# Performance work log

Hardware: AMD Instinct MI355X
Metric: run time of the kernel (lower is better)

Reference implementation:

```python
import jax, jax.numpy as jnp
import numpy as np
import math

D_MODEL = 768
N_HEADS = 12
B, L = 2, 2048
ALPHA = 0.3

def setup_inputs() -> dict:
    key = jax.random.key(0)
    ks = jax.random.split(key, 7)
    s = 0.02
    return {
        "x": jax.random.normal(ks[0], (B, L, D_MODEL), dtype=jnp.float32),
        "Wqkv_w": jax.random.normal(ks[1], (D_MODEL, 3 * D_MODEL), dtype=jnp.float32) * s,
        "Wqkv_b": jax.random.normal(ks[2], (3 * D_MODEL,), dtype=jnp.float32) * s,
        "sel_w": jax.random.normal(ks[3], (D_MODEL, 2), dtype=jnp.float32) * s,
        "sel_b": jax.random.normal(ks[4], (2,), dtype=jnp.float32) * s,
        "out_w": jax.random.normal(ks[5], (D_MODEL, D_MODEL), dtype=jnp.float32) * s,
        "out_b": jax.random.normal(ks[6], (D_MODEL,), dtype=jnp.float32) * s,
        "temperature": jnp.ones((1,), dtype=jnp.float32) * (math.sqrt(D_MODEL) * ALPHA),
    }

def reference(x, Wqkv_w, Wqkv_b, sel_w, sel_b, out_w, out_b, temperature):
    b, l, d = x.shape
    h = N_HEADS
    hd = d // h
    # QKV projection: (B, L, 3, H, hd)
    qkv = (x @ Wqkv_w + Wqkv_b).reshape(b, l, 3, h, hd)
    q, k_, v = qkv[:, :, 0], qkv[:, :, 1], qkv[:, :, 2]
    scale = 1.0 / math.sqrt(hd)
    scores = jnp.einsum('bthd,bshd->bhts', q, k_ * scale)  # (B,H,L,L)
    causal_mask = jnp.triu(jnp.full((l, l), -10000.0, dtype=scores.dtype), 1)
    attn = jax.nn.softmax(scores + causal_mask, axis=-1)
    ctx = jnp.einsum('bhts,bshd->bthd', attn, v).reshape(b, l, d)
    attn_output = ctx @ out_w + out_b  # (B,L,D)
    # selection gate: softmax over 2 logits, keep prob of class 1 -> (B,L,1)
    selection = jax.nn.softmax((x @ sel_w + sel_b) / temperature, axis=-1)[..., 1:]
    # eval-mode top-k routing
    k_sel = int(math.ceil(math.sqrt(l)))
    _, idx = jax.lax.top_k(selection[..., 0], k_sel)  # (B, k)
    gated = attn_output * selection  # (B,L,D)
    src = jnp.take_along_axis(gated, idx[..., None], axis=1)  # (B,k,D)
    y = jax.vmap(lambda xb, ib, sb: xb.at[ib].add(sb))(x, idx, src)
    return y
```

## Files before the change

kernel.cpp:

```cpp
#include <hip/hip_runtime.h>
#include <hip/hip_bf16.h>
#include <cstddef>

#define BATCH 2
#define SEQ   2048
#define DM    768
#define NH    12
#define HD    64
#define N3    2304
#define NKV   1536
#define KSEL  46
#define NROW  (BATCH*KSEL)
#define NCHUNK 32

typedef unsigned short ushort_t;
typedef __attribute__((ext_vector_type(8))) short bf16x8;
typedef __attribute__((ext_vector_type(4))) float f32x4;

__device__ __forceinline__ ushort_t f2bf(float f) {
  union { __hip_bfloat16 h; ushort_t u; } cv;
  cv.h = __float2bfloat16(f);
  return cv.u;
}
__device__ __forceinline__ float bf2f(ushort_t u) {
  union { unsigned int i; float f; } cv;
  cv.i = ((unsigned int)u) << 16;
  return cv.f;
}

#define GLD16(g, l)                                                         \
  __builtin_amdgcn_global_load_lds(                                         \
      (const __attribute__((address_space(1))) void*)(g),                   \
      (__attribute__((address_space(3))) void*)(l), 16, 0, 0)

__global__ __launch_bounds__(256) void prep_kernel(
    const float* __restrict__ x, const float* __restrict__ W,
    const float* __restrict__ Wo,
    const float* __restrict__ sel_w, const float* __restrict__ sel_b,
    const float* __restrict__ temp,
    ushort_t* __restrict__ xb, ushort_t* __restrict__ Wt,
    ushort_t* __restrict__ WoT,
    float* __restrict__ sel, float* __restrict__ y) {
  const int bx = blockIdx.x;
  const int tid = threadIdx.x;
  if (bx < 1024) {
    const int w = tid >> 6, lane = tid & 63;
    const int row = bx * 4 + w;
    const float4* xr4 = (const float4*)(x + (size_t)row * DM);
    float4* yr4 = (float4*)(y + (size_t)row * DM);
    ushort4* xb4 = (ushort4*)(xb + (size_t)row * DM);
    const float4* sw4 = (const float4*)sel_w;
    float a0 = 0.f, a1 = 0.f;
#pragma unroll
    for (int i = 0; i < 3; ++i) {
      const int p = i * 64 + lane;
      float4 f = xr4[p];
      yr4[p] = f;
      ushort4 o;
      o.x = f2bf(f.x); o.y = f2bf(f.y); o.z = f2bf(f.z); o.w = f2bf(f.w);
      xb4[p] = o;
      float4 sa = sw4[p * 2];
      float4 sb = sw4[p * 2 + 1];
      a0 += f.x * sa.x + f.y * sa.z + f.z * sb.x + f.w * sb.z;
      a1 += f.x * sa.y + f.y * sa.w + f.z * sb.y + f.w * sb.w;
    }
    for (int off = 32; off; off >>= 1) {
      a0 += __shfl_xor(a0, off);
      a1 += __shfl_xor(a1, off);
    }
    if (lane == 0) {
      float t = temp[0];
      float l0 = (a0 + sel_b[0]) / t;
      float l1 = (a1 + sel_b[1]) / t;
      sel[row] = 1.0f / (1.0f + expf(l0 - l1));
    }
  } else if (bx < 2752) {
    __shared__ float tile[32][33];
    const int bx2 = bx - 1024;
    const int n0 = (bx2 % 72) * 32, k0 = (bx2 / 72) * 32;
    const int r = tid >> 3, c4 = (tid & 7) * 4;
    float4 f = *(const float4*)&W[(size_t)(k0 + r) * N3 + n0 + c4];
    tile[r][c4] = f.x; tile[r][c4 + 1] = f.y; tile[r][c4 + 2] = f.z; tile[r][c4 + 3] = f.w;
    __syncthreads();
    ushort4 o;
    o.x = f2bf(tile[c4 + 0][r]);
    o.y = f2bf(tile[c4 + 1][r]);
    o.z = f2bf(tile[c4 + 2][r]);
    o.w = f2bf(tile[c4 + 3][r]);
    *(ushort4*)&Wt[(size_t)(n0 + r) * DM + k0 + c4] = o;
  } else {
    __shared__ float tile2[32][33];
    const int bx3 = bx - 2752;
    const int n0 = (bx3 % 24) * 32, k0 = (bx3 / 24) * 32;
    const int r = tid >> 3, c4 = (tid & 7) * 4;
    float4 f = *(const float4*)&Wo[(size_t)(k0 + r) * DM + n0 + c4];
    tile2[r][c4] = f.x; tile2[r][c4 + 1] = f.y; tile2[r][c4 + 2] = f.z; tile2[r][c4 + 3] = f.w;
    __syncthreads();
    ushort4 o;
    o.x = f2bf(tile2[c4 + 0][r]);
    o.y = f2bf(tile2[c4 + 1][r]);
    o.z = f2bf(tile2[c4 + 2][r]);
    o.w = f2bf(tile2[c4 + 3][r]);
    *(ushort4*)&WoT[(size_t)(n0 + r) * DM + k0 + c4] = o;
  }
}

__global__ __launch_bounds__(256) void topk_kernel(
    const float* __restrict__ sel, int* __restrict__ idx,
    int* __restrict__ idxp) {
  __shared__ unsigned int hist[256];
  __shared__ unsigned int cum[256];
  __shared__ unsigned int wtot[4];
  __shared__ int sh_b;
  __shared__ int c_gt, c_eq;
  __shared__ int tmp_gt[KSEL];
  __shared__ int eqlist[256];
  __shared__ int fin[64];
  __shared__ int srt[64];
  const int b = blockIdx.x, tid = threadIdx.x;
  const int lane = tid & 63, w = tid >> 6;

  unsigned int key[8];
  int  kidx[8];
#pragma unroll
  for (int e = 0; e < 8; ++e) {
    int i = e * 256 + tid;
    kidx[e] = i;
    key[e] = __float_as_uint(sel[b * SEQ + i]);
  }
  unsigned int prefix = 0, mask = 0;
  int r = KSEL;
#pragma unroll
  for (int p = 3; p >= 0; --p) {
    const int shift = 8 * p;
    hist[tid] = 0;
    __syncthreads();
#pragma unroll
    for (int e = 0; e < 8; ++e)
      if ((key[e] & mask) == prefix)
        atomicAdd(&hist[(key[e] >> shift) & 255], 1u);
    __syncthreads();
    unsigned int v = hist[tid];
#pragma unroll
    for (int off = 1; off < 64; off <<= 1) {
      unsigned int t = __shfl_down(v, off);
      if (lane + off < 64) v += t;
    }
    if (lane == 0) wtot[w] = v;
    __syncthreads();
    unsigned int addhi = 0;
    for (int ww = w + 1; ww < 4; ++ww) addhi += wtot[ww];
    v += addhi;
    cum[tid] = v;
    __syncthreads();
    if (v >= (unsigned int)r && (tid == 255 || cum[tid + 1] < (unsigned int)r))
      sh_b = tid;
    __syncthreads();
    const int bsel = sh_b;
    r -= (bsel == 255) ? 0 : (int)cum[bsel + 1];
    prefix |= ((unsigned int)bsel) << shift;
    mask |= 0xFFu << shift;
    __syncthreads();
  }
  if (tid == 0) { c_gt = 0; c_eq = 0; }
  __syncthreads();
#pragma unroll
  for (int e = 0; e < 8; ++e) {
    if (key[e] > prefix) {
      int pos = atomicAdd(&c_gt, 1);
      tmp_gt[pos] = kidx[e];
    } else if (key[e] == prefix) {
      int pos = atomicAdd(&c_eq, 1);
      if (pos < 256) eqlist[pos] = kidx[e];
    }
  }
  __syncthreads();
  if (tid == 0) {
    const int need = KSEL - c_gt;
    const int ec = (c_eq < 256) ? c_eq : 256;
    for (int a = 0; a < need; ++a) {
      int mb = a;
      for (int bb = a + 1; bb < ec; ++bb)
        if (eqlist[bb] < eqlist[mb]) mb = bb;
      int tv = eqlist[a]; eqlist[a] = eqlist[mb]; eqlist[mb] = tv;
    }
  }
  __syncthreads();
  if (tid < KSEL)
    fin[tid] = (tid < c_gt) ? tmp_gt[tid] : eqlist[tid - c_gt];
  __syncthreads();
  if (tid < KSEL) {
    const int v = fin[tid];
    int rank = 0;
    for (int j = 0; j < KSEL; ++j) rank += (fin[j] < v);
    srt[rank] = v;
  }
  __syncthreads();
  if (tid < 64) {
    if (tid < KSEL) {
      idx[b * KSEL + tid] = srt[tid];
      idxp[b * 64 + tid] = srt[tid];
    } else {
      idxp[b * 64 + tid] = 0;
    }
  }
}

__global__ __launch_bounds__(256) void gemm_kernel(
    const ushort_t* __restrict__ Xbf,
    const ushort_t* __restrict__ Wt,
    const float* __restrict__ bias,
    const int* __restrict__ idxp,
    ushort_t* __restrict__ Ckv,
    ushort_t* __restrict__ qb) {
  __shared__ ushort_t As[128 * 32];
  __shared__ ushort_t Bs[64 * 32];
  const int bid = blockIdx.x;
  const int tid = threadIdx.x;
  const int lane = tid & 63, w = tid >> 6;
  const int wr = w >> 1, wc = w & 1;
  const int quad = lane >> 4, l16 = lane & 15;
  const int ci0 = tid;
  const int ci1 = 256 + tid;
  const bool isQ = (bid >= 768);
  int m0, nw0;
  size_t ga0, ga1;
  if (isQ) {
    m0 = 0;
    nw0 = (bid - 768) * 64;
    const int r0 = ci0 >> 2, r1 = ci1 >> 2;
    ga0 = (size_t)((r0 >> 6) * SEQ + idxp[r0]) * DM;
    ga1 = (size_t)((r1 >> 6) * SEQ + idxp[r1]) * DM;
  } else {
    const int bid2 = (bid & 7) * 96 + (bid >> 3);
    m0 = (bid2 / 24) * 128;
    nw0 = 768 + (bid2 % 24) * 64;
    ga0 = (size_t)(m0 + (ci0 >> 2)) * DM;
    ga1 = (size_t)(m0 + (ci1 >> 2)) * DM;
  }
  const size_t gb0 = (size_t)(nw0 + (tid >> 2)) * DM;
  const int ka0 = (ci0 & 3) * 8, ka1 = (ci1 & 3) * 8;
  const int kq = (tid & 3) * 8;

  f32x4 acc[4][2] = {};
  for (int k0 = 0; k0 < DM; k0 += 32) {
    GLD16(Xbf + ga0 + k0 + ka0, &As[(w * 64) * 8]);
    GLD16(Xbf + ga1 + k0 + ka1, &As[(256 + w * 64) * 8]);
    GLD16(Wt + gb0 + k0 + kq, &Bs[(w * 16) * 32]);
    __syncthreads();
    bf16x8 af[4], bfr[2];
#pragma unroll
    for (int i = 0; i < 4; ++i)
      af[i] = *(const bf16x8*)&As[(wr * 64 + i * 16 + l16) * 32 + quad * 8];
#pragma unroll
    for (int j = 0; j < 2; ++j)
      bfr[j] = *(const bf16x8*)&Bs[(wc * 32 + j * 16 + l16) * 32 + quad * 8];
#pragma unroll
    for (int i = 0; i < 4; ++i)
#pragma unroll
      for (int j = 0; j < 2; ++j)
        acc[i][j] = __builtin_amdgcn_mfma_f32_16x16x32_bf16(af[i], bfr[j], acc[i][j], 0, 0, 0);
    __syncthreads();
  }
#pragma unroll
  for (int i = 0; i < 4; ++i) {
    const int row_base = wr * 64 + i * 16 + quad * 4;
#pragma unroll
    for (int j = 0; j < 2; ++j) {
      const int col = nw0 + wc * 32 + j * 16 + l16;
      const float bv = bias[col];
      if (isQ) {
#pragma unroll
        for (int r = 0; r < 4; ++r)
          qb[(size_t)(row_base + r) * DM + col] = f2bf(acc[i][j][r] + bv);
      } else {
#pragma unroll
        for (int r = 0; r < 4; ++r)
          Ckv[(size_t)(m0 + row_base + r) * NKV + (col - 768)] = f2bf(acc[i][j][r] + bv);
      }
    }
  }
}

__global__ __launch_bounds__(256) void attn_chunk_kernel(
    const ushort_t* __restrict__ kv,
    const ushort_t* __restrict__ qb,
    const int* __restrict__ idx,
    float* __restrict__ m_part, float* __restrict__ l_part,
    ushort_t* __restrict__ o_part) {
  __shared__ __align__(16) ushort_t Vt[64][72];
  __shared__ __align__(16) ushort_t Ps[4][16][72];
  __shared__ int tS[64];
  __shared__ int tmaxS;
  const int tid = threadIdx.x;
  const int c = blockIdx.x, h = blockIdx.y, b = blockIdx.z;
  const int c0 = c * 64;
  if (tid < 64) {
    int t = (tid < KSEL) ? idx[b * KSEL + tid] : -1;
    tS[tid] = t;
    int tm = t;
    for (int off = 32; off; off >>= 1) tm = max(tm, __shfl_xor(tm, off));
    if (tid == 0) tmaxS = tm;
  }
  __syncthreads();
  if (c0 > tmaxS) return;

  {
    const int key = tid >> 2, ds0 = (tid & 3) * 16;
    const ushort_t* vsrc = kv + (size_t)(b * SEQ + c0 + key) * NKV + DM + h * HD + ds0;
    ushort_t tmp[16];
    *(uint4*)&tmp[0] = *(const uint4*)&vsrc[0];
    *(uint4*)&tmp[8] = *(const uint4*)&vsrc[8];
#pragma unroll
    for (int i = 0; i < 16; ++i) Vt[ds0 + i][key] = tmp[i];
  }

  const int lane = tid & 63, w = tid >> 6;
  const int quad = lane >> 4, l16 = lane & 15;

  const ushort_t* qsrc = qb + (size_t)(b * 64 + w * 16 + l16) * DM + h * HD + quad * 8;
  bf16x8 aq0 = *(const bf16x8*)&qsrc[0];
  bf16x8 aq1 = *(const bf16x8*)&qsrc[32];

  f32x4 acc[4] = {};
#pragma unroll
  for (int nt = 0; nt < 4; ++nt) {
    const ushort_t* ksrc = kv + (size_t)(b * SEQ + c0 + nt * 16 + l16) * NKV + h * HD + quad * 8;
    bf16x8 bk0 = *(const bf16x8*)&ksrc[0];
    bf16x8 bk1 = *(const bf16x8*)&ksrc[32];
    acc[nt] = __builtin_amdgcn_mfma_f32_16x16x32_bf16(aq0, bk0, acc[nt], 0, 0, 0);
    acc[nt] = __builtin_amdgcn_mfma_f32_16x16x32_bf16(aq1, bk1, acc[nt], 0, 0, 0);
  }

  float p[4][4];
  float mrow[4], lrow[4];
#pragma unroll
  for (int r = 0; r < 4; ++r) {
    const int q = w * 16 + quad * 4 + r;
    const int t = tS[q];
    float mx = -1e30f;
#pragma unroll
    for (int nt = 0; nt < 4; ++nt) {
      float s = acc[nt][r] * 0.125f;
      if (c0 + nt * 16 + l16 > t) s = -1e30f;
      p[nt][r] = s;
      mx = fmaxf(mx, s);
    }
#pragma unroll
    for (int off = 1; off < 16; off <<= 1) mx = fmaxf(mx, __shfl_xor(mx, off));
    float sum = 0.f;
#pragma unroll
    for (int nt = 0; nt < 4; ++nt) {
      float pv = __expf(p[nt][r] - mx);
      p[nt][r] = pv;
      sum += pv;
    }
#pragma unroll
    for (int off = 1; off < 16; off <<= 1) sum += __shfl_xor(sum, off);
    mrow[r] = mx; lrow[r] = sum;
  }

  const size_t pbase = ((size_t)(b * NH + h) * NCHUNK + c) * 64;
  if (l16 == 0) {
#pragma unroll
    for (int r = 0; r < 4; ++r) {
      const int q = w * 16 + quad * 4 + r;
      m_part[pbase + q] = mrow[r];
      l_part[pbase + q] = lrow[r];
    }
  }

#pragma unroll
  for (int r = 0; r < 4; ++r)
#pragma unroll
    for (int nt = 0; nt < 4; ++nt)
      Ps[w][quad * 4 + r][nt * 16 + l16] = f2bf(p[nt][r]);
  __syncthreads();

  bf16x8 ap0 = *(const bf16x8*)&Ps[w][l16][quad * 8];
  bf16x8 ap1 = *(const bf16x8*)&Ps[w][l16][32 + quad * 8];
  f32x4 acc2[4] = {};
#pragma unroll
  for (int nt = 0; nt < 4; ++nt) {
    bf16x8 bv0 = *(const bf16x8*)&Vt[nt * 16 + l16][quad * 8];
    bf16x8 bv1 = *(const bf16x8*)&Vt[nt * 16 + l16][32 + quad * 8];
    acc2[nt] = __builtin_amdgcn_mfma_f32_16x16x32_bf16(ap0, bv0, acc2[nt], 0, 0, 0);
    acc2[nt] = __builtin_amdgcn_mfma_f32_16x16x32_bf16(ap1, bv1, acc2[nt], 0, 0, 0);
  }
  ushort_t* obp = o_part + pbase * 64;
#pragma unroll
  for (int nt = 0; nt < 4; ++nt)
#pragma unroll
    for (int r = 0; r < 4; ++r)
      obp[(w * 16 + quad * 4 + r) * 64 + nt * 16 + l16] = f2bf(acc2[nt][r]);
}

__global__ __launch_bounds__(256) void attn_combine_kernel(
    const float* __restrict__ m_part, const float* __restrict__ l_part,
    const ushort_t* __restrict__ o_part, const int* __restrict__ idx,
    ushort_t* __restrict__ ctx_bf) {
  __shared__ float wgt[NCHUNK][16];
  __shared__ float linv[16];
  __shared__ int ncS[16];
  const int rg = blockIdx.x, h = blockIdx.y, b = blockIdx.z;
  const int tid = threadIdx.x;
  const size_t base = (size_t)(b * NH + h) * NCHUNK * 64;
  if (tid < 16) {
    const int q = rg * 16 + tid;
    float L = 0.f; int nc = 0;
    if (q < KSEL) {
      const int t = idx[b * KSEL + q];
      nc = (t >> 6) + 1;
      float M = -1e30f;
      for (int cc = 0; cc < nc; ++cc)
        M = fmaxf(M, m_part[base + cc * 64 + q]);
      for (int cc = 0; cc < nc; ++cc) {
        float wv = __expf(m_part[base + cc * 64 + q] - M);
        wgt[cc][tid] = wv;
        L += wv * l_part[base + cc * 64 + q];
      }
    }
    ncS[tid] = nc;
    linv[tid] = (L > 0.f) ? 1.0f / L : 0.f;
  }
  __syncthreads();
  const int rl = tid >> 4;
  const int d4 = (tid & 15) * 4;
  const int q = rg * 16 + rl;
  if (q >= KSEL) return;
  const int nc = ncS[rl];
  float4 a = {0.f, 0.f, 0.f, 0.f};
  const ushort_t* obp = o_part + base * 64 + (size_t)q * 64 + d4;
  for (int cc = 0; cc < nc; ++cc) {
    const float wv = wgt[cc][rl];
    const ushort4 ov = *(const ushort4*)&obp[(size_t)cc * 4096];
    a.x += wv * bf2f(ov.x); a.y += wv * bf2f(ov.y);
    a.z += wv * bf2f(ov.z); a.w += wv * bf2f(ov.w);
  }
  const float li = linv[rl];
  ushort4 o;
  o.x = f2bf(a.x * li); o.y = f2bf(a.y * li);
  o.z = f2bf(a.z * li); o.w = f2bf(a.w * li);
  *(ushort4*)&ctx_bf[(size_t)(b * 64 + q) * DM + h * HD + d4] = o;
}

__global__ __launch_bounds__(256) void outproj_kernel(
    const ushort_t* __restrict__ ctx_bf,
    const ushort_t* __restrict__ WoT,
    const float* __restrict__ ob, const int* __restrict__ idx,
    const float* __restrict__ sel, float* __restrict__ y) {
  __shared__ ushort_t As[128 * 32];
  __shared__ ushort_t Bs[64 * 32];
  const int tid = threadIdx.x;
  const int lane = tid & 63, w = tid >> 6;
  const int wr = w >> 1, wc = w & 1;
  const int kb = blockIdx.x / 12;
  const int n0 = (blockIdx.x % 12) * 64;
  const int kbase = kb * 384;
  const int quad = lane >> 4, l16 = lane & 15;
  const int ci0 = tid;
  const int ci1 = 256 + tid;
  const size_t ga0 = (size_t)(ci0 >> 2) * DM;
  const size_t ga1 = (size_t)(ci1 >> 2) * DM;
  const size_t gb0 = (size_t)(n0 + (tid >> 2)) * DM;
  const int ka0 = (ci0 & 3) * 8, ka1 = (ci1 & 3) * 8;
  const int kq = (tid & 3) * 8;
  f32x4 acc[4][2] = {};
  for (int k0 = kbase; k0 < kbase + 384; k0 += 32) {
    GLD16(ctx_bf + ga0 + k0 + ka0, &As[(w * 64) * 8]);
    GLD16(ctx_bf + ga1 + k0 + ka1, &As[(256 + w * 64) * 8]);
    GLD16(WoT + gb0 + k0 + kq, &Bs[(w * 16) * 32]);
    __syncthreads();
    bf16x8 af[4], bfr[2];
#pragma unroll
    for (int i = 0; i < 4; ++i)
      af[i] = *(const bf16x8*)&As[(wr * 64 + i * 16 + l16) * 32 + quad * 8];
#pragma unroll
    for (int j = 0; j < 2; ++j)
      bfr[j] = *(const bf16x8*)&Bs[(wc * 32 + j * 16 + l16) * 32 + quad * 8];
#pragma unroll
    for (int i = 0; i < 4; ++i)
#pragma unroll
      for (int j = 0; j < 2; ++j)
        acc[i][j] = __builtin_amdgcn_mfma_f32_16x16x32_bf16(af[i], bfr[j], acc[i][j], 0, 0, 0);
    __syncthreads();
  }
#pragma unroll
  for (int i = 0; i < 4; ++i) {
#pragma unroll
    for (int r = 0; r < 4; ++r) {
      const int row = wr * 64 + i * 16 + quad * 4 + r;
      const int b = row >> 6, jj = row & 63;
      if (jj >= KSEL) continue;
      const int t = idx[b * KSEL + jj];
      const float sv = sel[b * SEQ + t];
      float* yr = y + (size_t)(b * SEQ + t) * DM;
#pragma unroll
      for (int j = 0; j < 2; ++j) {
        const int col = n0 + wc * 32 + j * 16 + l16;
        const float bv = (kb == 0) ? ob[col] : 0.f;
        atomicAdd(&yr[col], (acc[i][j][r] + bv) * sv);
      }
    }
  }
}

extern "C" void kernel_launch(void* const* d_in, const int* in_sizes, int n_in,
                              void* d_out, int out_size, void* d_ws, size_t ws_size,
                              hipStream_t stream) {
  const float* x      = (const float*)d_in[0];
  const float* Wqkv_w = (const float*)d_in[1];
  const float* Wqkv_b = (const float*)d_in[2];
  const float* sel_w  = (const float*)d_in[3];
  const float* sel_b  = (const float*)d_in[4];
  const float* out_w  = (const float*)d_in[5];
  const float* out_b  = (const float*)d_in[6];
  const float* temp   = (const float*)d_in[7];
  float* y = (float*)d_out;

  char* wsb = (char*)d_ws;
  ushort_t* kv     = (ushort_t*)wsb;  wsb += (size_t)BATCH * SEQ * NKV * 2;
  ushort_t* o_part = (ushort_t*)wsb;  wsb += (size_t)24 * NCHUNK * 64 * 64 * 2;
  float*    m_part = (float*)wsb;     wsb += (size_t)24 * NCHUNK * 64 * 4;
  float*    l_part = (float*)wsb;     wsb += (size_t)24 * NCHUNK * 64 * 4;
  float*    sel    = (float*)wsb;     wsb += (size_t)BATCH * SEQ * 4;
  int*      idx    = (int*)wsb;       wsb += 128 * 4;
  int*      idxp   = (int*)wsb;       wsb += 128 * 4;
  ushort_t* ctx_bf = (ushort_t*)wsb;  wsb += (size_t)128 * DM * 2;
  ushort_t* qb     = (ushort_t*)wsb;  wsb += (size_t)128 * DM * 2;
  ushort_t* Xbf    = (ushort_t*)wsb;  wsb += (size_t)BATCH * SEQ * DM * 2;
  ushort_t* Wt     = (ushort_t*)wsb;  wsb += (size_t)N3 * DM * 2;
  ushort_t* WoT    = (ushort_t*)wsb;  wsb += (size_t)DM * DM * 2;

  prep_kernel<<<dim3(3328), 256, 0, stream>>>(x, Wqkv_w, out_w, sel_w, sel_b, temp,
                                              Xbf, Wt, WoT, sel, y);
  topk_kernel<<<dim3(BATCH), 256, 0, stream>>>(sel, idx, idxp);
  gemm_kernel<<<dim3(780), 256, 0, stream>>>(Xbf, Wt, Wqkv_b, idxp, kv, qb);
  attn_chunk_kernel<<<dim3(NCHUNK, NH, BATCH), 256, 0, stream>>>(kv, qb, idx, m_part, l_part, o_part);
  attn_combine_kernel<<<dim3(3, NH, BATCH), 256, 0, stream>>>(m_part, l_part, o_part, idx, ctx_bf);
  outproj_kernel<<<dim3(6 * 4), 256, 0, stream>>>(ctx_bf, WoT, out_b, idx, sel, y);
}
```

Baseline: 156.9 us.

## Enlarge QKV GEMM tiles to 128x128x64 with XOR-swizzled LDS

```diff
diff --git a/kernel.cpp b/kernel.cpp
--- a/kernel.cpp
+++ b/kernel.cpp
@@ -213,61 +213,81 @@
     const int* __restrict__ idxp,
     ushort_t* __restrict__ Ckv,
     ushort_t* __restrict__ qb) {
-  __shared__ ushort_t As[128 * 32];
-  __shared__ ushort_t Bs[64 * 32];
+  __shared__ ushort_t As[128 * 64];
+  __shared__ ushort_t Bs[128 * 64];
   const int bid = blockIdx.x;
   const int tid = threadIdx.x;
   const int lane = tid & 63, w = tid >> 6;
   const int wr = w >> 1, wc = w & 1;
   const int quad = lane >> 4, l16 = lane & 15;
-  const int ci0 = tid;
-  const int ci1 = 256 + tid;
-  const bool isQ = (bid >= 768);
-  int m0, nw0;
-  size_t ga0, ga1;
+  const bool isQ = (bid >= 384);
+  int m0, n0;
+  int srow[4], scol[4];
+#pragma unroll
+  for (int j = 0; j < 4; ++j) {
+    const int chunk = (j * 4 + w) * 64 + lane;
+    srow[j] = chunk >> 3;
+    scol[j] = ((chunk & 7) ^ (srow[j] & 7)) * 8;
+  }
+  size_t gaRow[4], gbRow[4];
   if (isQ) {
     m0 = 0;
-    nw0 = (bid - 768) * 64;
-    const int r0 = ci0 >> 2, r1 = ci1 >> 2;
-    ga0 = (size_t)((r0 >> 6) * SEQ + idxp[r0]) * DM;
-    ga1 = (size_t)((r1 >> 6) * SEQ + idxp[r1]) * DM;
+    n0 = (bid - 384) * 128;
+#pragma unroll
+    for (int j = 0; j < 4; ++j)
+      gaRow[j] = (size_t)((srow[j] >> 6) * SEQ + idxp[srow[j]]) * DM;
   } else {
-    const int bid2 = (bid & 7) * 96 + (bid >> 3);
-    m0 = (bid2 / 24) * 128;
-    nw0 = 768 + (bid2 % 24) * 64;
-    ga0 = (size_t)(m0 + (ci0 >> 2)) * DM;
-    ga1 = (size_t)(m0 + (ci1 >> 2)) * DM;
-  }
-  const size_t gb0 = (size_t)(nw0 + (tid >> 2)) * DM;
-  const int ka0 = (ci0 & 3) * 8, ka1 = (ci1 & 3) * 8;
-  const int kq = (tid & 3) * 8;
-
-  f32x4 acc[4][2] = {};
-  for (int k0 = 0; k0 < DM; k0 += 32) {
-    GLD16(Xbf + ga0 + k0 + ka0, &As[(w * 64) * 8]);
-    GLD16(Xbf + ga1 + k0 + ka1, &As[(256 + w * 64) * 8]);
-    GLD16(Wt + gb0 + k0 + kq, &Bs[(w * 16) * 32]);
-    __syncthreads();
-    bf16x8 af[4], bfr[2];
+    const int bid2 = (bid & 7) * 48 + (bid >> 3);
+    m0 = (bid2 / 12) * 128;
+    n0 = 768 + (bid2 % 12) * 128;
+#pragma unroll
+    for (int j = 0; j < 4; ++j)
+      gaRow[j] = (size_t)(m0 + srow[j]) * DM;
+  }
+#pragma unroll
+  for (int j = 0; j < 4; ++j)
+    gbRow[j] = (size_t)(n0 + srow[j]) * DM;
+
+  f32x4 acc[4][4] = {};
+  for (int k0 = 0; k0 < DM; k0 += 64) {
+#pragma unroll
+    for (int j = 0; j < 4; ++j) {
+      GLD16(Xbf + gaRow[j] + k0 + scol[j], &As[(j * 4 + w) * 512]);
+      GLD16(Wt + gbRow[j] + k0 + scol[j], &Bs[(j * 4 + w) * 512]);
+    }
+    __syncthreads();
+    bf16x8 af[4][2], bfr[4][2];
+#pragma unroll
+    for (int i = 0; i < 4; ++i) {
+      const int row = wr * 64 + i * 16 + l16;
+      const int sw = row & 7;
+#pragma unroll
+      for (int ks = 0; ks < 2; ++ks)
+        af[i][ks] = *(const bf16x8*)&As[row * 64 + (((quad + ks * 4) ^ sw) * 8)];
+    }
+#pragma unroll
+    for (int j2 = 0; j2 < 4; ++j2) {
+      const int row = wc * 64 + j2 * 16 + l16;
+      const int sw = row & 7;
+#pragma unroll
+      for (int ks = 0; ks < 2; ++ks)
+        bfr[j2][ks] = *(const bf16x8*)&Bs[row * 64 + (((quad + ks * 4) ^ sw) * 8)];
+    }
 #pragma unroll
     for (int i = 0; i < 4; ++i)
-      af[i] = *(const bf16x8*)&As[(wr * 64 + i * 16 + l16) * 32 + quad * 8];
-#pragma unroll
-    for (int j = 0; j < 2; ++j)
-      bfr[j] = *(const bf16x8*)&Bs[(wc * 32 + j * 16 + l16) * 32 + quad * 8];
-#pragma unroll
-    for (int i = 0; i < 4; ++i)
-#pragma unroll
-      for (int j = 0; j < 2; ++j)
-        acc[i][j] = __builtin_amdgcn_mfma_f32_16x16x32_bf16(af[i], bfr[j], acc[i][j], 0, 0, 0);
+#pragma unroll
+      for (int j2 = 0; j2 < 4; ++j2) {
+        acc[i][j2] = __builtin_amdgcn_mfma_f32_16x16x32_bf16(af[i][0], bfr[j2][0], acc[i][j2], 0, 0, 0);
+        acc[i][j2] = __builtin_amdgcn_mfma_f32_16x16x32_bf16(af[i][1], bfr[j2][1], acc[i][j2], 0, 0, 0);
+      }
     __syncthreads();
   }
 #pragma unroll
   for (int i = 0; i < 4; ++i) {
     const int row_base = wr * 64 + i * 16 + quad * 4;
 #pragma unroll
-    for (int j = 0; j < 2; ++j) {
-      const int col = nw0 + wc * 32 + j * 16 + l16;
+    for (int j = 0; j < 4; ++j) {
+      const int col = n0 + wc * 64 + j * 16 + l16;
       const float bv = bias[col];
       if (isQ) {
 #pragma unroll
@@ -535,7 +555,7 @@
   prep_kernel<<<dim3(3328), 256, 0, stream>>>(x, Wqkv_w, out_w, sel_w, sel_b, temp,
                                               Xbf, Wt, WoT, sel, y);
   topk_kernel<<<dim3(BATCH), 256, 0, stream>>>(sel, idx, idxp);
-  gemm_kernel<<<dim3(780), 256, 0, stream>>>(Xbf, Wt, Wqkv_b, idxp, kv, qb);
+  gemm_kernel<<<dim3(390), 256, 0, stream>>>(Xbf, Wt, Wqkv_b, idxp, kv, qb);
   attn_chunk_kernel<<<dim3(NCHUNK, NH, BATCH), 256, 0, stream>>>(kv, qb, idx, m_part, l_part, o_part);
   attn_combine_kernel<<<dim3(3, NH, BATCH), 256, 0, stream>>>(m_part, l_part, o_part, idx, ctx_bf);
   outproj_kernel<<<dim3(6 * 4), 256, 0, stream>>>(ctx_bf, WoT, out_b, idx, sel, y);
```

Measured after the change: 152.8 us. 2.6% less time.
